# Kernel optimization log

Measured on AMD Instinct MI355X. Metric: run time of the kernel, lower is better.

## Reference

```python
import jax, jax.numpy as jnp
import numpy as np
from jax import lax


def setup_inputs() -> dict:
    key = jax.random.key(0)
    k1, k2, k3 = jax.random.split(key, 3)
    B, C, H, W = 16, 64, 128, 128
    Hc = 64
    x = jax.random.normal(k1, (B, C, H, W), dtype=jnp.float32)
    # Conv2d(in=C, out=4*Hc, kernel=(3,1)) weight [O, I, kH, kW] and bias
    fan_in = C * 3 * 1
    bound = 1.0 / np.sqrt(fan_in)
    conv_w = jax.random.uniform(k2, (4 * Hc, C, 3, 1), dtype=jnp.float32, minval=-bound, maxval=bound)
    conv_b = jax.random.uniform(k3, (4 * Hc,), dtype=jnp.float32, minval=-bound, maxval=bound)
    return {"x": x, "conv_w": conv_w, "conv_b": conv_b}


def reference(x, conv_w, conv_b):
    # Gates depend only on x, so run the causal (3,1) conv once over the full image.
    # Top-pad height by 2 (matches F.pad(col, (0,0,2,0)) per column in the original).
    gates = lax.conv_general_dilated(
        x, conv_w,
        window_strides=(1, 1),
        padding=[(2, 0), (0, 0)],
        dimension_numbers=("NCHW", "OIHW", "NCHW"),
    ) + conv_b[None, :, None, None]            # [B, 4*Hc, H, W]

    i, f, o, g = jnp.split(gates, 4, axis=1)   # each [B, Hc, H, W]
    i = jax.nn.sigmoid(i)
    f = jax.nn.sigmoid(f)
    o = jax.nn.sigmoid(o)
    g = jnp.tanh(g)

    # Scan the LSTM cell recurrence over the width dimension.
    # Move W to the leading axis: [W, B, Hc, H]
    seq = tuple(jnp.moveaxis(t, 3, 0) for t in (i, f, o, g))
    Hc = i.shape[1]
    c0 = jnp.zeros((x.shape[0], Hc, x.shape[2]), dtype=x.dtype)

    def step(c, ifog):
        i_t, f_t, o_t, g_t = ifog
        c = f_t * c + i_t * g_t
        h = o_t * jnp.tanh(c)
        return c, h

    _, hs = lax.scan(step, c0, seq)            # hs: [W, B, Hc, H]
    return jnp.moveaxis(hs, 0, 3)              # [B, Hc, H, W]
```

## Files before the change

kernel.cpp:

```cpp
#include <hip/hip_runtime.h>


#define NB   16
#define NC   64
#define NH   128
#define NW   128
#define NHC  64
#define NK   192
#define NPLN (NB * NH * NW * NHC)

typedef _Float16 half4 __attribute__((ext_vector_type(4)));
typedef _Float16 half8 __attribute__((ext_vector_type(8)));
typedef float    f32x4 __attribute__((ext_vector_type(4)));

__device__ __forceinline__ float fsig(float x)  { return 1.f / (1.f + __expf(-x)); }
__device__ __forceinline__ float ftanh(float x) { return 1.f - 2.f / (__expf(2.f * x) + 1.f); }

#define NIP 3088

__global__ __launch_bounds__(256, 2) void gates_k(
    const float* __restrict__ x,
    const float* __restrict__ wgt,
    const float* __restrict__ bias,
    _Float16* __restrict__ fpl,
    _Float16* __restrict__ ppl,
    _Float16* __restrict__ opl)
{
    __shared__ _Float16 xsf[8 * NIP];

    const int tid  = threadIdx.x;
    const int cg   = tid >> 6;
    const int lane = tid & 63;
    const int l15  = lane & 15;
    const int l4   = lane >> 4;

    int bid = blockIdx.x;
    bid = (bid & 7) * (NB * NH / 8) + (bid >> 3);
    const int b = bid >> 7;
    const int h = bid & (NH - 1);

    const float* xb = x + (size_t)b * NC * NH * NW;

    half8 afrag[4][6];
    #pragma unroll
    for (int g = 0; g < 4; ++g) {
        const float* wo = wgt + (size_t)(g * 64 + cg * 16 + l15) * NK;
        #pragma unroll
        for (int kt = 0; kt < 6; ++kt) {
            const float4 v0 = *(const float4*)(wo + kt * 32 + l4 * 8);
            const float4 v1 = *(const float4*)(wo + kt * 32 + l4 * 8 + 4);
            half8 a;
            a[0] = (_Float16)v0.x; a[1] = (_Float16)v0.y;
            a[2] = (_Float16)v0.z; a[3] = (_Float16)v0.w;
            a[4] = (_Float16)v1.x; a[5] = (_Float16)v1.y;
            a[6] = (_Float16)v1.z; a[7] = (_Float16)v1.w;
            afrag[g][kt] = a;
        }
    }
    float bfr[4][4];
    #pragma unroll
    for (int g = 0; g < 4; ++g)
        #pragma unroll
        for (int j = 0; j < 4; ++j)
            bfr[g][j] = bias[g * 64 + cg * 16 + l4 * 4 + j];

    for (int t = tid; t < 1536; t += 256) {
        const int kq  = t >> 5;
        const int wq  = t & 31;
        const int k0  = kq * 4;
        const int w0g = wq * 4;
        float4 v[4];
        #pragma unroll
        for (int dk = 0; dk < 4; ++dk) {
            const int k  = k0 + dk;
            const int c  = k / 3;
            const int kh = k - 3 * c;
            const int r  = h - 2 + kh;
            v[dk] = (r >= 0) ? *(const float4*)(xb + ((size_t)c * NH + r) * NW + w0g)
                             : make_float4(0.f, 0.f, 0.f, 0.f);
        }
        const int kt = k0 >> 5;
        const int j0 = k0 & 7;
        #pragma unroll
        for (int dw = 0; dw < 4; ++dw) {
            const int w  = w0g + dw;
            const int ni = w >> 4;
            const int L  = ((k0 & 31) >> 3) * 16 + (w & 15);
            half4 hv;
            hv[0] = (_Float16)(&v[0].x)[dw];
            hv[1] = (_Float16)(&v[1].x)[dw];
            hv[2] = (_Float16)(&v[2].x)[dw];
            hv[3] = (_Float16)(&v[3].x)[dw];
            *(half4*)&xsf[ni * NIP + kt * 512 + L * 8 + j0] = hv;
        }
    }
    __syncthreads();

    #pragma unroll
    for (int pr = 0; pr < 4; ++pr) {
        f32x4 acc[4][2];
        #pragma unroll
        for (int g = 0; g < 4; ++g) {
            acc[g][0] = (f32x4){0.f, 0.f, 0.f, 0.f};
            acc[g][1] = (f32x4){0.f, 0.f, 0.f, 0.f};
        }
        #pragma unroll
        for (int kt = 0; kt < 6; ++kt) {
            const half8 b0 = *(const half8*)&xsf[(pr * 2 + 0) * NIP + kt * 512 + lane * 8];
            const half8 b1 = *(const half8*)&xsf[(pr * 2 + 1) * NIP + kt * 512 + lane * 8];
            #pragma unroll
            for (int g = 0; g < 4; ++g) {
                acc[g][0] = __builtin_amdgcn_mfma_f32_16x16x32_f16(afrag[g][kt], b0, acc[g][0], 0, 0, 0);
                acc[g][1] = __builtin_amdgcn_mfma_f32_16x16x32_f16(afrag[g][kt], b1, acc[g][1], 0, 0, 0);
            }
        }
        #pragma unroll
        for (int q = 0; q < 2; ++q) {
            const int w   = (pr * 2 + q) * 16 + l15;
            const int hc0 = cg * 16 + l4 * 4;
            half4 f4, p4, o4;
            #pragma unroll
            for (int j = 0; j < 4; ++j) {
                const float iv = fsig (acc[0][q][j] + bfr[0][j]);
                const float fv = fsig (acc[1][q][j] + bfr[1][j]);
                const float ov = fsig (acc[2][q][j] + bfr[2][j]);
                const float gv = ftanh(acc[3][q][j] + bfr[3][j]);
                f4[j] = (_Float16)fv;
                p4[j] = (_Float16)(iv * gv);
                o4[j] = (_Float16)ov;
            }
            const size_t sb = (((size_t)(b * NH + h) * NW) + w) * NHC + hc0;
            *(half4*)(fpl + sb) = f4;
            *(half4*)(ppl + sb) = p4;
            *(half4*)(opl + sb) = o4;
        }
    }
}

__global__ __launch_bounds__(256) void scan_k(
    const _Float16* __restrict__ fpl,
    const _Float16* __restrict__ ppl,
    const _Float16* __restrict__ opl,
    float* __restrict__ out)
{
    __shared__ float hbuf[4][NHC][33];

    const int tid  = threadIdx.x;
    const int wv   = tid >> 6;
    const int lane = tid & 63;
    const int row  = blockIdx.x * 4 + wv;
    const int b    = row >> 7;
    const int h    = row & (NH - 1);

    const size_t gbase = ((size_t)(b * NH + h) * NW) * NHC + lane;
    float c = 0.f;

    for (int ck = 0; ck < 4; ++ck) {
        const size_t p0 = gbase + (size_t)ck * 32 * NHC;
        #pragma unroll
        for (int s = 0; s < 32; ++s) {
            const size_t ix = p0 + (size_t)s * NHC;
            const float f = (float)fpl[ix];
            const float p = (float)ppl[ix];
            const float o = (float)opl[ix];
            c = fmaf(f, c, p);
            hbuf[wv][lane][s] = o * ftanh(c);
        }
        const int wl = lane & 31;
        const int hq = lane >> 5;
        #pragma unroll
        for (int it = 0; it < 32; ++it) {
            const int hc = it * 2 + hq;
            out[(((size_t)b * NHC + hc) * NH + h) * NW + ck * 32 + wl] = hbuf[wv][hc][wl];
        }
    }
}

#define WC 32
#define GP (WC + 2)
#define NQ (48 * WC)
__device__ __forceinline__ void stage_chunk_fb(const float* __restrict__ xb, int h, int w0,
                                               _Float16 (*xsf)[6][64][8], int qstart, int qstep) {
    for (int q = qstart; q < NQ; q += qstep) {
        const int k4 = q >> 5; const int w = q & 31;
        const int ni = w >> 4; const int kt = k4 >> 3;
        const int L = ((k4 >> 1) & 3) * 16 + (w & 15);
        const int j0 = (k4 & 1) * 4;
        half4 hv;
        #pragma unroll
        for (int e = 0; e < 4; ++e) {
            const int k = k4 * 4 + e; const int c = k / 3;
            const int kh = k - 3 * c; const int r = h - 2 + kh;
            float v = 0.f;
            if (r >= 0) v = xb[((size_t)c * NH + r) * NW + w0 + w];
            hv[e] = (_Float16)v;
        }
        *(half4*)&xsf[ni][kt][L][j0] = hv;
    }
}
__global__ __launch_bounds__(256, 2) void rowlstm_fb(
    const float* __restrict__ x, const float* __restrict__ wgt,
    const float* __restrict__ bias, float* __restrict__ out)
{
    __shared__ _Float16 xsf[2][6][64][8];
    __shared__ float fbuf[NHC][GP]; __shared__ float pbuf[NHC][GP]; __shared__ float obuf[NHC][GP];
    const int tid = threadIdx.x; const int cg = tid >> 6;
    const int lane = tid & 63; const int l15 = lane & 15; const int l4 = lane >> 4;
    int bid = blockIdx.x; bid = (bid & 7) * (NB * NH / 8) + (bid >> 3);
    const int b = bid >> 7; const int h = bid & (NH - 1);
    const float* xb = x + (size_t)b * NC * NH * NW;
    half8 afrag[4][6];
    #pragma unroll
    for (int g = 0; g < 4; ++g) {
        const float* wo = wgt + (size_t)(g * 64 + cg * 16 + l15) * NK;
        #pragma unroll
        for (int kt = 0; kt < 6; ++kt) {
            const float4 v0 = *(const float4*)(wo + kt * 32 + l4 * 8);
            const float4 v1 = *(const float4*)(wo + kt * 32 + l4 * 8 + 4);
            half8 a;
            a[0]=(_Float16)v0.x;a[1]=(_Float16)v0.y;a[2]=(_Float16)v0.z;a[3]=(_Float16)v0.w;
            a[4]=(_Float16)v1.x;a[5]=(_Float16)v1.y;a[6]=(_Float16)v1.z;a[7]=(_Float16)v1.w;
            afrag[g][kt] = a;
        }
    }
    float bfr[4][4];
    #pragma unroll
    for (int g = 0; g < 4; ++g)
        #pragma unroll
        for (int j = 0; j < 4; ++j) bfr[g][j] = bias[g * 64 + cg * 16 + l4 * 4 + j];
    float cstate = 0.f;
    float* outrow = out + (((size_t)b * NHC + tid) * NH + h) * NW;
    stage_chunk_fb(xb, h, 0, xsf, tid, 256);
    __syncthreads();
    for (int ck = 0; ck < 4; ++ck) {
        const int w0 = ck * WC;
        f32x4 acc[4][2];
        #pragma unroll
        for (int g = 0; g < 4; ++g) { acc[g][0]=(f32x4){0,0,0,0}; acc[g][1]=(f32x4){0,0,0,0}; }
        #pragma unroll
        for (int kt = 0; kt < 6; ++kt) {
            const half8 b0 = *(const half8*)&xsf[0][kt][lane][0];
            const half8 b1 = *(const half8*)&xsf[1][kt][lane][0];
            #pragma unroll
            for (int g = 0; g < 4; ++g) {
                acc[g][0] = __builtin_amdgcn_mfma_f32_16x16x32_f16(afrag[g][kt], b0, acc[g][0], 0, 0, 0);
                acc[g][1] = __builtin_amdgcn_mfma_f32_16x16x32_f16(afrag[g][kt], b1, acc[g][1], 0, 0, 0);
            }
        }
        #pragma unroll
        for (int ni = 0; ni < 2; ++ni)
            #pragma unroll
            for (int j = 0; j < 4; ++j) {
                const float iv = fsig (acc[0][ni][j] + bfr[0][j]);
                const float fv = fsig (acc[1][ni][j] + bfr[1][j]);
                const float ov = fsig (acc[2][ni][j] + bfr[2][j]);
                const float gv = ftanh(acc[3][ni][j] + bfr[3][j]);
                const int hcr = cg * 16 + l4 * 4 + j; const int wcl = ni * 16 + l15;
                fbuf[hcr][wcl] = fv; pbuf[hcr][wcl] = iv * gv; obuf[hcr][wcl] = ov;
            }
        __syncthreads();
        if (tid < 64) {
            float c = cstate;
            #pragma unroll
            for (int w = 0; w < WC; w += 4) {
                float4 hv;
                #pragma unroll
                for (int e = 0; e < 4; ++e) {
                    c = fmaf(fbuf[tid][w + e], c, pbuf[tid][w + e]);
                    (&hv.x)[e] = obuf[tid][w + e] * ftanh(c);
                }
                *(float4*)(outrow + w0 + w) = hv;
            }
            cstate = c;
        } else if (ck < 3) stage_chunk_fb(xb, h, w0 + WC, xsf, tid - 64, 192);
        __syncthreads();
    }
}

extern "C" void kernel_launch(void* const* d_in, const int* in_sizes, int n_in,
                              void* d_out, int out_size, void* d_ws, size_t ws_size,
                              hipStream_t stream) {
    const float* x    = (const float*)d_in[0];
    const float* wgt  = (const float*)d_in[1];
    const float* bias = (const float*)d_in[2];
    float* out = (float*)d_out;

    if (ws_size >= (size_t)3 * NPLN * sizeof(_Float16)) {
        _Float16* fpl = (_Float16*)d_ws;
        _Float16* ppl = fpl + NPLN;
        _Float16* opl = ppl + NPLN;
        gates_k<<<NB * NH, 256, 0, stream>>>(x, wgt, bias, fpl, ppl, opl);
        scan_k<<<NB * NH / 4, 256, 0, stream>>>(fpl, ppl, opl, out);
    } else {
        rowlstm_fb<<<NB * NH, 256, 0, stream>>>(x, wgt, bias, out);
    }
}
```

Before: 254.8 us.

## Pack f and i*g into one plane, prefetch scan inputs, use fast reciprocal

Interleaves the forget gate and the i*g product as half2 pairs in one 32-bit plane, so the scan does one load per step for those two values instead of two. The scan is restructured into double-buffered register prefetch of 16-step blocks, with vectorized float2 output stores and a padded LDS buffer. Sigmoid and tanh now use the hardware reciprocal builtin instead of division, and the gates kernel's launch bound asks for 3 blocks per SM. The faster reciprocal loses a little accuracy, and the larger prefetch arrays raise register pressure in the scan.

```diff
diff --git a/kernel.cpp b/kernel.cpp
--- a/kernel.cpp
+++ b/kernel.cpp
@@ -13,18 +13,18 @@
 typedef _Float16 half8 __attribute__((ext_vector_type(8)));
 typedef float    f32x4 __attribute__((ext_vector_type(4)));
 
-__device__ __forceinline__ float fsig(float x)  { return 1.f / (1.f + __expf(-x)); }
-__device__ __forceinline__ float ftanh(float x) { return 1.f - 2.f / (__expf(2.f * x) + 1.f); }
+__device__ __forceinline__ float frcp(float x)  { return __builtin_amdgcn_rcpf(x); }
+__device__ __forceinline__ float fsig(float x)  { return frcp(1.f + __expf(-x)); }
+__device__ __forceinline__ float ftanh(float x) { return 1.f - 2.f * frcp(__expf(2.f * x) + 1.f); }
 
 #define NIP 3088
 
-__global__ __launch_bounds__(256, 2) void gates_k(
+__global__ __launch_bounds__(256, 3) void gates_k(
     const float* __restrict__ x,
     const float* __restrict__ wgt,
     const float* __restrict__ bias,
-    _Float16* __restrict__ fpl,
-    _Float16* __restrict__ ppl,
-    _Float16* __restrict__ opl)
+    uint32_t*  __restrict__ fppl,
+    _Float16*  __restrict__ opl)
 {
     __shared__ _Float16 xsf[8 * NIP];
 
@@ -118,32 +118,33 @@
         for (int q = 0; q < 2; ++q) {
             const int w   = (pr * 2 + q) * 16 + l15;
             const int hc0 = cg * 16 + l4 * 4;
-            half4 f4, p4, o4;
+            uint32_t fp4[4];
+            half4 o4;
             #pragma unroll
             for (int j = 0; j < 4; ++j) {
                 const float iv = fsig (acc[0][q][j] + bfr[0][j]);
                 const float fv = fsig (acc[1][q][j] + bfr[1][j]);
                 const float ov = fsig (acc[2][q][j] + bfr[2][j]);
                 const float gv = ftanh(acc[3][q][j] + bfr[3][j]);
-                f4[j] = (_Float16)fv;
-                p4[j] = (_Float16)(iv * gv);
-                o4[j] = (_Float16)ov;
-            }
-            const size_t sb = (((size_t)(b * NH + h) * NW) + w) * NHC + hc0;
-            *(half4*)(fpl + sb) = f4;
-            *(half4*)(ppl + sb) = p4;
-            *(half4*)(opl + sb) = o4;
+                union { _Float16 h[2]; uint32_t u; } pk;
+                pk.h[0] = (_Float16)fv;
+                pk.h[1] = (_Float16)(iv * gv);
+                fp4[j] = pk.u;
+                o4[j]  = (_Float16)ov;
+            }
+            const size_t eb = ((size_t)(b * NH + h) * NW + w) * NHC + hc0;
+            *(uint4*)(fppl + eb) = make_uint4(fp4[0], fp4[1], fp4[2], fp4[3]);
+            *(half4*)(opl  + eb) = o4;
         }
     }
 }
 
 __global__ __launch_bounds__(256) void scan_k(
-    const _Float16* __restrict__ fpl,
-    const _Float16* __restrict__ ppl,
+    const uint32_t* __restrict__ fppl,
     const _Float16* __restrict__ opl,
     float* __restrict__ out)
 {
-    __shared__ float hbuf[4][NHC][33];
+    __shared__ float hbuf[4][NHC][34];
 
     const int tid  = threadIdx.x;
     const int wv   = tid >> 6;
@@ -152,28 +153,52 @@
     const int b    = row >> 7;
     const int h    = row & (NH - 1);
 
-    const size_t gbase = ((size_t)(b * NH + h) * NW) * NHC + lane;
-    float c = 0.f;
-
-    for (int ck = 0; ck < 4; ++ck) {
-        const size_t p0 = gbase + (size_t)ck * 32 * NHC;
-        #pragma unroll
-        for (int s = 0; s < 32; ++s) {
-            const size_t ix = p0 + (size_t)s * NHC;
-            const float f = (float)fpl[ix];
-            const float p = (float)ppl[ix];
-            const float o = (float)opl[ix];
-            c = fmaf(f, c, p);
-            hbuf[wv][lane][s] = o * ftanh(c);
-        }
-        const int wl = lane & 31;
-        const int hq = lane >> 5;
-        #pragma unroll
-        for (int it = 0; it < 32; ++it) {
-            const int hc = it * 2 + hq;
-            out[(((size_t)b * NHC + hc) * NH + h) * NW + ck * 32 + wl] = hbuf[wv][hc][wl];
-        }
-    }
+    const size_t base = ((size_t)(b * NH + h) * NW) * NHC + lane;
+    const uint32_t* fpp = fppl + base;
+    const _Float16* opp = opl  + base;
+    float* outb = out + (size_t)b * NHC * NH * NW;
+    float* hrow = &hbuf[wv][lane][0];
+
+    uint32_t fA[16], fB[16];
+    _Float16 oA[16], oB[16];
+
+#define LOAD16(FP, OV, W0)                                     \
+    _Pragma("unroll")                                          \
+    for (int s = 0; s < 16; ++s) {                             \
+        FP[s] = fpp[(size_t)((W0) + s) * NHC];                 \
+        OV[s] = opp[(size_t)((W0) + s) * NHC];                 \
+    }
+
+#define STEP(FPV, OV, WIDX) {                                  \
+        union { uint32_t u; _Float16 hh[2]; } pk; pk.u = (FPV);\
+        const float fv = (float)pk.hh[0];                      \
+        const float pv = (float)pk.hh[1];                      \
+        cst = fmaf(fv, cst, pv);                               \
+        hrow[WIDX] = (float)(OV) * ftanh(cst); }
+
+    float cst = 0.f;
+    LOAD16(fA, oA, 0);
+
+    #pragma unroll
+    for (int pair = 0; pair < 4; ++pair) {
+        const int w0 = pair * 32;
+        LOAD16(fB, oB, w0 + 16);
+        #pragma unroll
+        for (int s = 0; s < 16; ++s) STEP(fA[s], oA[s], s);
+        if (pair < 3) { LOAD16(fA, oA, w0 + 32); }
+        #pragma unroll
+        for (int s = 0; s < 16; ++s) STEP(fB[s], oB[s], 16 + s);
+
+        #pragma unroll
+        for (int it = 0; it < 16; ++it) {
+            const int hc = it * 4 + (lane >> 4);
+            const int wl = (lane & 15) * 2;
+            const float2 v = *(const float2*)&hbuf[wv][hc][wl];
+            *(float2*)(outb + ((size_t)hc * NH + h) * NW + w0 + wl) = v;
+        }
+    }
+#undef LOAD16
+#undef STEP
 }
 
 #define WC 32
@@ -286,11 +311,10 @@
     float* out = (float*)d_out;
 
     if (ws_size >= (size_t)3 * NPLN * sizeof(_Float16)) {
-        _Float16* fpl = (_Float16*)d_ws;
-        _Float16* ppl = fpl + NPLN;
-        _Float16* opl = ppl + NPLN;
-        gates_k<<<NB * NH, 256, 0, stream>>>(x, wgt, bias, fpl, ppl, opl);
-        scan_k<<<NB * NH / 4, 256, 0, stream>>>(fpl, ppl, opl, out);
+        uint32_t* fppl = (uint32_t*)d_ws;
+        _Float16* opl  = (_Float16*)d_ws + (size_t)2 * NPLN;
+        gates_k<<<NB * NH, 256, 0, stream>>>(x, wgt, bias, fppl, opl);
+        scan_k<<<NB * NH / 4, 256, 0, stream>>>(fppl, opl, out);
     } else {
         rowlstm_fb<<<NB * NH, 256, 0, stream>>>(x, wgt, bias, out);
     }
```

Measured after the change: 317.6 us. 1.25x slower.
